# Optimization experiments

Hardware: AMD Instinct MI355X
Metric: run time of the kernel (lower is better)

The kernel has to match this reference:

```python
import jax, jax.numpy as jnp
import numpy as np

DIM = 768
NUM_HEADS = 12
HEAD_DIM = DIM // NUM_HEADS
HW = 32  # input_size = (32, 32)


def setup_inputs() -> dict:
    key = jax.random.key(0)
    ks = jax.random.split(key, 7)
    return {
        "x": jax.random.normal(ks[0], (8, HW, HW, DIM), dtype=jnp.float32),
        "w_qkv": jax.random.normal(ks[1], (DIM, 3 * DIM), dtype=jnp.float32) * 0.02,
        "b_qkv": jnp.zeros((3 * DIM,), dtype=jnp.float32),
        "w_proj": jax.random.normal(ks[2], (DIM, DIM), dtype=jnp.float32) * 0.02,
        "b_proj": jnp.zeros((DIM,), dtype=jnp.float32),
        "rel_pos_h": jax.random.normal(ks[3], (2 * HW - 1, HEAD_DIM), dtype=jnp.float32) * 0.02,
        "rel_pos_w": jax.random.normal(ks[4], (2 * HW - 1, HEAD_DIM), dtype=jnp.float32) * 0.02,
    }


def _gather_rel_pos(size, rel_pos):
    # q_size == k_size == size, so no resize; index = i - j + (size - 1)
    idx = jnp.arange(size)[:, None] - jnp.arange(size)[None, :] + (size - 1)
    return rel_pos[idx]  # [size, size, head_dim]


def reference(x, w_qkv, b_qkv, w_proj, b_proj, rel_pos_h, rel_pos_w):
    B, H, W, C = x.shape
    nH, D = NUM_HEADS, HEAD_DIM
    scale = D ** -0.5
    S = H * W

    qkv = x.reshape(B, S, C) @ w_qkv + b_qkv          # [B,S,3C]
    qkv = qkv.reshape(B, S, 3, nH, D).transpose(2, 0, 3, 1, 4)  # [3,B,nH,S,D]
    q, k, v = qkv[0], qkv[1], qkv[2]

    attn = jnp.einsum('bnsd,bntd->bnst', q * scale, k)  # [B,nH,S,S]

    # decomposed relative positional bias
    Rh = _gather_rel_pos(H, rel_pos_h)                  # [H,H,D]
    Rw = _gather_rel_pos(W, rel_pos_w)                  # [W,W,D]
    r_q = q.reshape(B, nH, H, W, D)
    rel_h = jnp.einsum('bnhwc,hkc->bnhwk', r_q, Rh)     # [B,nH,H,W,H]
    rel_w = jnp.einsum('bnhwc,wkc->bnhwk', r_q, Rw)     # [B,nH,H,W,W]
    attn = (attn.reshape(B, nH, H, W, H, W)
            + rel_h[..., :, None]
            + rel_w[..., None, :]).reshape(B, nH, S, S)

    attn = jax.nn.softmax(attn, axis=-1)
    out = jnp.einsum('bnst,bntd->bnsd', attn, v)        # [B,nH,S,D]
    out = out.transpose(0, 2, 1, 3).reshape(B, H, W, C)
    return out @ w_proj + b_proj
```

## Files before the change

kernel.cpp:

```cpp
#include <hip/hip_runtime.h>
#include <cstdint>
#include <cstddef>

#define NH 12
#define HDIM 64
#define C_ 768
#define C3 2304
#define SEQ 1024
#define LS 72
#define LSV 76
#define SMAX 6.0f
#define LOG2E 1.4426950408889634f

typedef short bf16x8_t __attribute__((ext_vector_type(8)));
typedef float f32x4_t __attribute__((ext_vector_type(4)));
typedef unsigned short u16x4_t __attribute__((ext_vector_type(4)));

__device__ __forceinline__ unsigned short bf16_rne(float x) {
    unsigned int u = __float_as_uint(x);
    u += 0x7FFFu + ((u >> 16) & 1u);
    return (unsigned short)(u >> 16);
}
__device__ __forceinline__ float bf16f(unsigned short h) {
    return __uint_as_float(((unsigned int)h) << 16);
}

__device__ __forceinline__ void load_lds16(const unsigned short* g, unsigned short* l) {
    auto gp = (const __attribute__((address_space(1))) unsigned short*)(uintptr_t)g;
    auto lp = (__attribute__((address_space(3))) unsigned short*)(uint32_t)(uintptr_t)l;
    __builtin_amdgcn_global_load_lds(gp, lp, 16, 0, 0);
}

__device__ __forceinline__ int swz(int row, int g) {
    const int pr = row >> 1;
    const int ch = (((row & 1) << 2) | g) ^ (pr & 7);
    return pr * 64 + ch * 8;
}

__global__ __launch_bounds__(256)
void split_kernel(const float* __restrict__ in, unsigned short* __restrict__ hi)
{
    const int i = blockIdx.x * 256 + threadIdx.x;
    float4 v = ((const float4*)in)[i];
    u16x4_t h;
    h.x = bf16_rne(v.x); h.y = bf16_rne(v.y); h.z = bf16_rne(v.z); h.w = bf16_rne(v.w);
    ((u16x4_t*)hi)[i] = h;
}

__global__ __launch_bounds__(256)
void splitT_kernel(const float* __restrict__ W, unsigned short* __restrict__ Thi,
                   unsigned short* __restrict__ Tlo, int Kdim, int Ndim)
{
    __shared__ float tile[32][33];
    const int t = threadIdx.x;
    const int kb = blockIdx.y * 32, nb = blockIdx.x * 32;
    const int lr = t >> 3, lc = (t & 7) * 4;
    *(float4*)&tile[lr][lc] = *(const float4*)&W[(size_t)(kb + lr) * Ndim + nb + lc];
    __syncthreads();
    const float v0 = tile[lc + 0][lr];
    const float v1 = tile[lc + 1][lr];
    const float v2 = tile[lc + 2][lr];
    const float v3 = tile[lc + 3][lr];
    u16x4_t h, l;
    h.x = bf16_rne(v0); l.x = bf16_rne(v0 - bf16f(h.x));
    h.y = bf16_rne(v1); l.y = bf16_rne(v1 - bf16f(h.y));
    h.z = bf16_rne(v2); l.z = bf16_rne(v2 - bf16f(h.z));
    h.w = bf16_rne(v3); l.w = bf16_rne(v3 - bf16f(h.w));
    *(u16x4_t*)&Thi[(size_t)(nb + lr) * Kdim + kb + lc] = h;
    *(u16x4_t*)&Tlo[(size_t)(nb + lr) * Kdim + kb + lc] = l;
}

__global__ __launch_bounds__(256, 4)
void qkvgemm_kernel(const unsigned short* __restrict__ Ahi, const unsigned short* __restrict__ BThi,
                    const float* __restrict__ bias,
                    unsigned short* __restrict__ q_hi, unsigned short* __restrict__ k_hi,
                    unsigned short* __restrict__ v_hi)
{
    constexpr int K = 768;
    __shared__ unsigned short As[2][4096];
    __shared__ unsigned short Bs[2][4096];
    const int tid = threadIdx.x;
    const int w = tid >> 6, lane = tid & 63, g = lane >> 4, r = lane & 15;
    const int wr = (w >> 1) * 64, wc = (w & 1) * 64;

    const int bid  = blockIdx.x;
    const int xcd  = bid & 7;
    const int idx  = bid >> 3;
    const int msub = idx & 7;
    const int ntile = idx >> 3;
    const int m0 = (xcd * 8 + msub) * 128;
    const int n0 = ntile * 128;

    int row_[2], gc_[2];
#pragma unroll
    for (int i = 0; i < 2; ++i) {
        const int s = i * 256 + tid;
        const int pr = s >> 3;
        const int u = (s & 7) ^ (pr & 7);
        row_[i] = pr * 2 + (u >> 2);
        gc_[i]  = u & 3;
    }
    const unsigned short* gA0 = Ahi + (size_t)(m0 + row_[0]) * K + gc_[0] * 8;
    const unsigned short* gA1 = Ahi + (size_t)(m0 + row_[1]) * K + gc_[1] * 8;
    const unsigned short* gB0 = BThi + (size_t)(n0 + row_[0]) * K + gc_[0] * 8;
    const unsigned short* gB1 = BThi + (size_t)(n0 + row_[1]) * K + gc_[1] * 8;
    const int lofs0 = w * 512;
    const int lofs1 = 2048 + w * 512;

    f32x4_t acc[4][4];
#pragma unroll
    for (int i = 0; i < 4; ++i)
#pragma unroll
        for (int j = 0; j < 4; ++j)
#pragma unroll
            for (int q = 0; q < 4; ++q) acc[i][j][q] = 0.f;

    load_lds16(gA0, &As[0][lofs0]);
    load_lds16(gA1, &As[0][lofs1]);
    load_lds16(gB0, &Bs[0][lofs0]);
    load_lds16(gB1, &Bs[0][lofs1]);

    int cur = 0;
    for (int k0 = 0; k0 < K; k0 += 32) {
        __syncthreads();
        if (k0 + 32 < K) {
            const int nb2 = cur ^ 1;
            load_lds16(gA0 + k0 + 32, &As[nb2][lofs0]);
            load_lds16(gA1 + k0 + 32, &As[nb2][lofs1]);
            load_lds16(gB0 + k0 + 32, &Bs[nb2][lofs0]);
            load_lds16(gB1 + k0 + 32, &Bs[nb2][lofs1]);
        }
        bf16x8_t am[4];
#pragma unroll
        for (int i = 0; i < 4; ++i)
            am[i] = *(const bf16x8_t*)&As[cur][swz(wr + 16 * i + r, g)];
#pragma unroll
        for (int j = 0; j < 4; ++j) {
            const bf16x8_t bn = *(const bf16x8_t*)&Bs[cur][swz(wc + 16 * j + r, g)];
#pragma unroll
            for (int i = 0; i < 4; ++i)
                acc[i][j] = __builtin_amdgcn_mfma_f32_16x16x32_bf16(am[i], bn, acc[i][j], 0, 0, 0);
        }
        cur ^= 1;
    }

    const int third = n0 >= 1536 ? 2 : (n0 >= 768 ? 1 : 0);
    unsigned short* outH = third == 2 ? v_hi : third == 1 ? k_hi : q_hi;
#pragma unroll
    for (int j = 0; j < 4; ++j) {
        const int n = n0 + wc + 16 * j + r;
        const float bj = bias[n];
        const int nn = n - third * 768;
        const int h = nn >> 6, d = nn & 63;
#pragma unroll
        for (int i = 0; i < 4; ++i) {
            const int m = m0 + wr + 16 * i + 4 * g;
            const int b = m >> 10, t = m & 1023;
            const size_t hb = ((size_t)(b * NH + h)) << 16;
            unsigned short* dh = outH + hb + (size_t)t * 64 + d;
#pragma unroll
            for (int q = 0; q < 4; ++q)
                dh[(size_t)q * 64] = bf16_rne(acc[i][j][q] + bj);
        }
    }
}

template<int N>
__global__ __launch_bounds__(256, 2)
void gemm_mfma_kernel(const unsigned short* __restrict__ Ahi, const unsigned short* __restrict__ Alo,
                      const unsigned short* __restrict__ BThi, const unsigned short* __restrict__ BTlo,
                      const float* __restrict__ bias, float* __restrict__ C)
{
    constexpr int K = 768;
    __shared__ unsigned short As[128 * LS];
    __shared__ unsigned short Bs[128 * LS];
    const int tid = threadIdx.x;
    const int w = tid >> 6, lane = tid & 63, g = lane >> 4, r = lane & 15;
    const int wr = (w >> 1) * 64, wc = (w & 1) * 64;

    const int bid  = blockIdx.x;
    const int xcd  = bid & 7;
    const int idx  = bid >> 3;
    const int msub = idx & 7;
    const int ntile = idx >> 3;
    const int m0 = (xcd * 8 + msub) * 128;
    const int n0 = ntile * 128;

    const int srow = tid >> 1, sh = (tid & 1) * 16;

    const unsigned short* aH = Ahi + (size_t)(m0 + srow) * K + sh;
    const unsigned short* aL = Alo + (size_t)(m0 + srow) * K + sh;
    const unsigned short* bH = BThi + (size_t)(n0 + srow) * K + sh;
    const unsigned short* bL = BTlo + (size_t)(n0 + srow) * K + sh;

    f32x4_t acc[4][4];
#pragma unroll
    for (int i = 0; i < 4; ++i)
#pragma unroll
        for (int j = 0; j < 4; ++j)
#pragma unroll
            for (int q = 0; q < 4; ++q) acc[i][j][q] = 0.f;

    for (int k0 = 0; k0 < K; k0 += 32) {
        bf16x8_t va0 = *(const bf16x8_t*)(aH + k0);
        bf16x8_t va1 = *(const bf16x8_t*)(aH + k0 + 8);
        bf16x8_t wa0 = *(const bf16x8_t*)(aL + k0);
        bf16x8_t wa1 = *(const bf16x8_t*)(aL + k0 + 8);
        bf16x8_t vb0 = *(const bf16x8_t*)(bH + k0);
        bf16x8_t vb1 = *(const bf16x8_t*)(bH + k0 + 8);
        bf16x8_t wb0 = *(const bf16x8_t*)(bL + k0);
        bf16x8_t wb1 = *(const bf16x8_t*)(bL + k0 + 8);
        __syncthreads();
        *(bf16x8_t*)&As[srow * LS + sh]          = va0;
        *(bf16x8_t*)&As[srow * LS + sh + 8]      = va1;
        *(bf16x8_t*)&As[srow * LS + 32 + sh]     = wa0;
        *(bf16x8_t*)&As[srow * LS + 32 + sh + 8] = wa1;
        *(bf16x8_t*)&Bs[srow * LS + sh]          = vb0;
        *(bf16x8_t*)&Bs[srow * LS + sh + 8]      = vb1;
        *(bf16x8_t*)&Bs[srow * LS + 32 + sh]     = wb0;
        *(bf16x8_t*)&Bs[srow * LS + 32 + sh + 8] = wb1;
        __syncthreads();
        bf16x8_t amh[4], aml[4];
#pragma unroll
        for (int i = 0; i < 4; ++i) {
            amh[i] = *(const bf16x8_t*)&As[(wr + 16 * i + r) * LS + 8 * g];
            aml[i] = *(const bf16x8_t*)&As[(wr + 16 * i + r) * LS + 32 + 8 * g];
        }
#pragma unroll
        for (int j = 0; j < 4; ++j) {
            bf16x8_t bnh = *(const bf16x8_t*)&Bs[(wc + 16 * j + r) * LS + 8 * g];
            bf16x8_t bnl = *(const bf16x8_t*)&Bs[(wc + 16 * j + r) * LS + 32 + 8 * g];
#pragma unroll
            for (int i = 0; i < 4; ++i) {
                acc[i][j] = __builtin_amdgcn_mfma_f32_16x16x32_bf16(amh[i], bnh, acc[i][j], 0, 0, 0);
                acc[i][j] = __builtin_amdgcn_mfma_f32_16x16x32_bf16(amh[i], bnl, acc[i][j], 0, 0, 0);
                acc[i][j] = __builtin_amdgcn_mfma_f32_16x16x32_bf16(aml[i], bnh, acc[i][j], 0, 0, 0);
            }
        }
    }

#pragma unroll
    for (int j = 0; j < 4; ++j) {
        const float bj = bias[n0 + wc + 16 * j + r];
#pragma unroll
        for (int i = 0; i < 4; ++i) {
            float* Cp = C + (size_t)(m0 + wr + 16 * i + 4 * g) * N + n0 + wc + 16 * j + r;
#pragma unroll
            for (int q = 0; q < 4; ++q)
                Cp[(size_t)q * N] = acc[i][j][q] + bj;
        }
    }
}

__global__ __launch_bounds__(256)
void relcat_kernel(const float* __restrict__ rel_h, const float* __restrict__ rel_w,
                   unsigned short* __restrict__ relcat)
{
    const int i = blockIdx.x * 256 + threadIdx.x;
    if (i >= 2016) return;
    const int j = i * 4;
    const int row = j >> 6, col = j & 63;
    const float* src = row < 63 ? &rel_h[row * 64 + col] : &rel_w[(row - 63) * 64 + col];
    const float4 v = *(const float4*)src;
    u16x4_t h;
    h.x = bf16_rne(v.x); h.y = bf16_rne(v.y); h.z = bf16_rne(v.z); h.w = bf16_rne(v.w);
    *(u16x4_t*)&relcat[j] = h;
}

__global__ __launch_bounds__(256, 4)
void relgemm_kernel(const unsigned short* __restrict__ qhi, const unsigned short* __restrict__ relcat,
                    unsigned short* __restrict__ G)
{
    __shared__ unsigned short bs[128 * LS];
    const int tid = threadIdx.x;
    const int sb = blockIdx.x, bh = blockIdx.y;
    const int w = tid >> 6, lane = tid & 63, g = lane >> 4, r = lane & 15;
    const size_t hb = (size_t)bh << 16;

    {
        const int row = tid >> 1, c32 = (tid & 1) * 32;
        if (row < 126) {
#pragma unroll
            for (int e = 0; e < 4; ++e)
                *(bf16x8_t*)&bs[row * LS + c32 + 8 * e] =
                    *(const bf16x8_t*)&relcat[row * 64 + c32 + 8 * e];
        } else {
            const bf16x8_t z = {0,0,0,0,0,0,0,0};
#pragma unroll
            for (int e = 0; e < 4; ++e)
                *(bf16x8_t*)&bs[row * LS + c32 + 8 * e] = z;
        }
    }
    bf16x8_t aq[2][2];
#pragma unroll
    for (int i = 0; i < 2; ++i)
#pragma unroll
        for (int c = 0; c < 2; ++c)
            aq[i][c] = *(const bf16x8_t*)(qhi + hb + (size_t)(sb * 128 + w * 32 + 16 * i + r) * 64 + c * 32 + 8 * g);
    __syncthreads();

    f32x4_t acc[2][8];
#pragma unroll
    for (int i = 0; i < 2; ++i)
#pragma unroll
        for (int fj = 0; fj < 8; ++fj)
#pragma unroll
            for (int q = 0; q < 4; ++q) acc[i][fj][q] = 0.f;

#pragma unroll
    for (int c = 0; c < 2; ++c)
#pragma unroll
        for (int fj = 0; fj < 8; ++fj) {
            const bf16x8_t brel = *(const bf16x8_t*)&bs[(16 * fj + r) * LS + c * 32 + 8 * g];
#pragma unroll
            for (int i = 0; i < 2; ++i)
                acc[i][fj] = __builtin_amdgcn_mfma_f32_16x16x32_bf16(aq[i][c], brel, acc[i][fj], 0, 0, 0);
        }

    unsigned short* Gb = G + (((size_t)bh << 10) + sb * 128 + w * 32) * 128;
#pragma unroll
    for (int i = 0; i < 2; ++i)
#pragma unroll
        for (int reg = 0; reg < 4; ++reg) {
            unsigned short* Gr = Gb + (size_t)(16 * i + 4 * g + reg) * 128 + r;
#pragma unroll
            for (int fj = 0; fj < 8; ++fj)
                Gr[16 * fj] = bf16_rne(acc[i][fj][reg]);
        }
}

__global__ __launch_bounds__(256, 4)
void attn10_kernel(const unsigned short* __restrict__ qhi,
                   const unsigned short* __restrict__ khi,
                   const unsigned short* __restrict__ vhi,
                   const unsigned short* __restrict__ G,
                   unsigned short* __restrict__ outh, unsigned short* __restrict__ outl)
{
    __shared__ unsigned short ksh[2 * 64 * LS];
    __shared__ unsigned short vsh[2 * 64 * LSV];

    const int tid  = threadIdx.x;
    const int bh   = blockIdx.x;
    const int s0   = blockIdx.y * 64;
    const int w    = tid >> 6;
    const int lane = tid & 63;
    const int g    = lane >> 4;
    const int r    = lane & 15;
    const size_t hb = (size_t)bh << 16;

    bf16x8_t aq[2];
#pragma unroll
    for (int c = 0; c < 2; ++c)
        aq[c] = *(const bf16x8_t*)(qhi + hb + (size_t)(s0 + w * 16 + r) * 64 + c * 32 + 8 * g);

    const unsigned short* Gbh = G + ((size_t)bh << 17);
    const int q    = s0 + w * 16 + r;
    const int qoff = q * 128;
    const int qcb  = (q >> 5) + 31;
    const int iw   = q & 31;
    float bw[4][2];
#pragma unroll
    for (int reg = 0; reg < 4; ++reg)
#pragma unroll
        for (int jh = 0; jh < 2; ++jh)
            bw[reg][jh] = bf16f(Gbh[qoff + 94 + iw - 16 * jh - 4 * g - reg]) * LOG2E;

    f32x4_t oacc[4];
    float lsum[4];
#pragma unroll
    for (int i = 0; i < 4; ++i) {
        lsum[i] = 0.f;
#pragma unroll
        for (int j = 0; j < 4; ++j) oacc[i][j] = 0.f;
    }

    const int krow = tid >> 2, kc16 = (tid & 3) * 16;
    const int tb = (tid >> 4) * 4, d0 = (tid & 15) * 4;
    const int addr_a = (((g & 1) << 5) + r) << 2;
    const int addr_b = addr_a + 64;
    const bool lowg = g < 2;

    {
        const unsigned short* kh = khi + hb + (size_t)krow * 64 + kc16;
        const bf16x8_t a0 = *(const bf16x8_t*)kh;
        const bf16x8_t a1 = *(const bf16x8_t*)(kh + 8);
        u16x4_t rv[4];
#pragma unroll
        for (int i = 0; i < 4; ++i)
            rv[i] = *(const u16x4_t*)(vhi + hb + (size_t)(tb + i) * 64 + d0);
        *(bf16x8_t*)&ksh[krow * LS + kc16]     = a0;
        *(bf16x8_t*)&ksh[krow * LS + kc16 + 8] = a1;
#pragma unroll
        for (int c2 = 0; c2 < 4; ++c2) {
            u16x4_t th;
            th.x = rv[0][c2]; th.y = rv[1][c2]; th.z = rv[2][c2]; th.w = rv[3][c2];
            *(u16x4_t*)&vsh[(d0 + c2) * LSV + tb] = th;
        }
    }
    __syncthreads();

    int cur = 0;
    for (int t0 = 0; t0 < SEQ; t0 += 64) {
        const int cok = cur * 64 * LS;
        const int cov = cur * 64 * LSV;
        const int tn = (t0 + 64 < SEQ) ? t0 + 64 : t0;
        bf16x8_t nk0, nk1;
        u16x4_t nv[4];
        {
            const unsigned short* kh = khi + hb + (size_t)(tn + krow) * 64 + kc16;
            nk0 = *(const bf16x8_t*)kh;
            nk1 = *(const bf16x8_t*)(kh + 8);
#pragma unroll
            for (int i = 0; i < 4; ++i)
                nv[i] = *(const u16x4_t*)(vhi + hb + (size_t)(tn + tb + i) * 64 + d0);
        }

        f32x4_t sacc[4];
#pragma unroll
        for (int fj = 0; fj < 4; ++fj)
#pragma unroll
            for (int j = 0; j < 4; ++j) sacc[fj][j] = 0.f;
#pragma unroll
        for (int c = 0; c < 2; ++c)
#pragma unroll
            for (int fj = 0; fj < 4; ++fj) {
                const bf16x8_t bkh = *(const bf16x8_t*)&ksh[cok + (16 * fj + r) * LS + c * 32 + 8 * g];
                sacc[fj] = __builtin_amdgcn_mfma_f32_16x16x32_bf16(bkh, aq[c], sacc[fj], 0, 0, 0);
            }

        const int kh0 = t0 >> 5;
        const float bh0 = (bf16f(Gbh[qoff + qcb - kh0])     - SMAX) * LOG2E;
        const float bh1 = (bf16f(Gbh[qoff + qcb - kh0 - 1]) - SMAX) * LOG2E;
#pragma unroll
        for (int fj = 0; fj < 4; ++fj)
#pragma unroll
            for (int reg = 0; reg < 4; ++reg) {
                const float s = fmaf(sacc[fj][reg], 0.125f * LOG2E,
                                     ((fj >> 1) ? bh1 : bh0) + bw[reg][fj & 1]);
                const float e = exp2f(s);
                sacc[fj][reg] = e;
                lsum[reg] += e;
            }

        unsigned int pk01[4], pk23[4];
#pragma unroll
        for (int fj = 0; fj < 4; ++fj) {
            asm("v_cvt_pk_bf16_f32 %0, %1, %2" : "=v"(pk01[fj]) : "v"(sacc[fj][0]), "v"(sacc[fj][1]));
            asm("v_cvt_pk_bf16_f32 %0, %1, %2" : "=v"(pk23[fj]) : "v"(sacc[fj][2]), "v"(sacc[fj][3]));
        }

#pragma unroll
        for (int c = 0; c < 2; ++c) {
            const int a01A = __builtin_amdgcn_ds_bpermute(addr_a, (int)pk01[2 * c]);
            const int a23A = __builtin_amdgcn_ds_bpermute(addr_a, (int)pk23[2 * c]);
            const int b01A = __builtin_amdgcn_ds_bpermute(addr_b, (int)pk01[2 * c]);
            const int b23A = __builtin_amdgcn_ds_bpermute(addr_b, (int)pk23[2 * c]);
            const int a01B = __builtin_amdgcn_ds_bpermute(addr_a, (int)pk01[2 * c + 1]);
            const int a23B = __builtin_amdgcn_ds_bpermute(addr_a, (int)pk23[2 * c + 1]);
            const int b01B = __builtin_amdgcn_ds_bpermute(addr_b, (int)pk01[2 * c + 1]);
            const int b23B = __builtin_amdgcn_ds_bpermute(addr_b, (int)pk23[2 * c + 1]);
            union { int u[4]; bf16x8_t v; } pf;
            pf.u[0] = lowg ? a01A : a01B;
            pf.u[1] = lowg ? a23A : a23B;
            pf.u[2] = lowg ? b01A : b01B;
            pf.u[3] = lowg ? b23A : b23B;
#pragma unroll
            for (int fd = 0; fd < 4; ++fd) {
                const bf16x8_t bvh = *(const bf16x8_t*)&vsh[cov + (16 * fd + r) * LSV + c * 32 + 8 * g];
                oacc[fd] = __builtin_amdgcn_mfma_f32_16x16x32_bf16(bvh, pf.v, oacc[fd], 0, 0, 0);
            }
        }

        const int nok = (cur ^ 1) * 64 * LS;
        const int nov = (cur ^ 1) * 64 * LSV;
        *(bf16x8_t*)&ksh[nok + krow * LS + kc16]     = nk0;
        *(bf16x8_t*)&ksh[nok + krow * LS + kc16 + 8] = nk1;
#pragma unroll
        for (int c2 = 0; c2 < 4; ++c2) {
            u16x4_t th;
            th.x = nv[0][c2]; th.y = nv[1][c2]; th.z = nv[2][c2]; th.w = nv[3][c2];
            *(u16x4_t*)&vsh[nov + (d0 + c2) * LSV + tb] = th;
        }
        __syncthreads();
        cur ^= 1;
    }

    const int b = bh / NH, h = bh - (bh / NH) * NH;
    float rs = (lsum[0] + lsum[1]) + (lsum[2] + lsum[3]);
    rs += __shfl_xor(rs, 16);
    rs += __shfl_xor(rs, 32);
    const float rinv = 1.f / rs;
    unsigned short* oph = outh + ((size_t)b * SEQ + q) * C_ + h * HDIM + 4 * g;
    unsigned short* opl = outl + ((size_t)b * SEQ + q) * C_ + h * HDIM + 4 * g;
#pragma unroll
    for (int fd = 0; fd < 4; ++fd) {
        u16x4_t hv, lv;
#pragma unroll
        for (int reg = 0; reg < 4; ++reg) {
            const float v = oacc[fd][reg] * rinv;
            const unsigned short hh = bf16_rne(v);
            hv[reg] = hh;
            lv[reg] = bf16_rne(v - bf16f(hh));
        }
        *(u16x4_t*)(oph + 16 * fd) = hv;
        *(u16x4_t*)(opl + 16 * fd) = lv;
    }
}

extern "C" void kernel_launch(void* const* d_in, const int* in_sizes, int n_in,
                              void* d_out, int out_size, void* d_ws, size_t ws_size,
                              hipStream_t stream) {
    (void)in_sizes; (void)n_in; (void)out_size; (void)ws_size;
    const float* x      = (const float*)d_in[0];
    const float* w_qkv  = (const float*)d_in[1];
    const float* b_qkv  = (const float*)d_in[2];
    const float* w_proj = (const float*)d_in[3];
    const float* b_proj = (const float*)d_in[4];
    const float* rel_h  = (const float*)d_in[5];
    const float* rel_w  = (const float*)d_in[6];
    float* out = (float*)d_out;

    char* base = (char*)d_ws;
    unsigned short* xhi    = (unsigned short*)(base + 0);
    unsigned short* xlo    = (unsigned short*)(base + 12582912);
    unsigned short* wqh    = (unsigned short*)(base + 25165824);
    unsigned short* wql    = (unsigned short*)(base + 28704768);
    unsigned short* wph    = (unsigned short*)(base + 32243712);
    unsigned short* wpl    = (unsigned short*)(base + 33423360);
    unsigned short* qhi    = (unsigned short*)(base + 34603008);
    unsigned short* relcat = (unsigned short*)(base + 47185920);
    unsigned short* khi    = (unsigned short*)(base + 59768832);
    unsigned short* vhi    = (unsigned short*)(base + 84934656);
    unsigned short* G      = (unsigned short*)(base + 110100480);
    unsigned short* ohif   = xhi;
    unsigned short* olo    = xlo;

    split_kernel<<<6144, 256, 0, stream>>>(x, xhi);
    {
        dim3 gq(C3 / 32, C_ / 32);
        splitT_kernel<<<gq, 256, 0, stream>>>(w_qkv, wqh, wql, C_, C3);
        dim3 gp(C_ / 32, C_ / 32);
        splitT_kernel<<<gp, 256, 0, stream>>>(w_proj, wph, wpl, C_, C_);
        relcat_kernel<<<8, 256, 0, stream>>>(rel_h, rel_w, relcat);
    }
    qkvgemm_kernel<<<1152, 256, 0, stream>>>(xhi, wqh, b_qkv, qhi, khi, vhi);
    {
        dim3 grid(8, 96);
        relgemm_kernel<<<grid, 256, 0, stream>>>(qhi, relcat, G);
    }
    {
        dim3 grid(96, SEQ / 64);
        attn10_kernel<<<grid, 256, 0, stream>>>(qhi, khi, vhi, G, ohif, olo);
    }
    gemm_mfma_kernel<C_><<<384, 256, 0, stream>>>(ohif, olo, wph, wpl, b_proj, out);
}
```

Before: 175.7 us.

## Fuse prep kernels, double-buffer proj GEMM with async LDS loads, add setprio

Merges the four preprocessing kernels (x bf16 cast, two weight split-transposes, rel-pos concat) into one launch dispatched by block index, removing three launch gaps. The projection GEMM switches from register-staged single-buffered LDS to double-buffered global_load_lds with the swizzled layout used by the QKV GEMM, so the next K tile loads while MFMAs run. s_setprio is raised around the MFMA blocks in the QKV GEMM, attention and projection kernels. The costs are higher LDS use in the projection GEMM, which may lower occupancy, and more divergent block roles in the prep kernel.

Result: faster. 166.8 us (-5.0%).

```diff
diff --git a/kernel.cpp b/kernel.cpp
--- a/kernel.cpp
+++ b/kernel.cpp
@@ -37,23 +37,12 @@
     return pr * 64 + ch * 8;
 }
 
-__global__ __launch_bounds__(256)
-void split_kernel(const float* __restrict__ in, unsigned short* __restrict__ hi)
+__device__ __forceinline__ void splitT_body(const float* __restrict__ W,
+                                            unsigned short* __restrict__ Thi,
+                                            unsigned short* __restrict__ Tlo,
+                                            int Kdim, int Ndim, int kb, int nb,
+                                            float (*tile)[33], int t)
 {
-    const int i = blockIdx.x * 256 + threadIdx.x;
-    float4 v = ((const float4*)in)[i];
-    u16x4_t h;
-    h.x = bf16_rne(v.x); h.y = bf16_rne(v.y); h.z = bf16_rne(v.z); h.w = bf16_rne(v.w);
-    ((u16x4_t*)hi)[i] = h;
-}
-
-__global__ __launch_bounds__(256)
-void splitT_kernel(const float* __restrict__ W, unsigned short* __restrict__ Thi,
-                   unsigned short* __restrict__ Tlo, int Kdim, int Ndim)
-{
-    __shared__ float tile[32][33];
-    const int t = threadIdx.x;
-    const int kb = blockIdx.y * 32, nb = blockIdx.x * 32;
     const int lr = t >> 3, lc = (t & 7) * 4;
     *(float4*)&tile[lr][lc] = *(const float4*)&W[(size_t)(kb + lr) * Ndim + nb + lc];
     __syncthreads();
@@ -70,6 +59,45 @@
     *(u16x4_t*)&Tlo[(size_t)(nb + lr) * Kdim + kb + lc] = l;
 }
 
+__global__ __launch_bounds__(256)
+void prep_kernel(const float* __restrict__ x, const float* __restrict__ w_qkv,
+                 const float* __restrict__ w_proj,
+                 const float* __restrict__ rel_h, const float* __restrict__ rel_w,
+                 unsigned short* __restrict__ xhi,
+                 unsigned short* __restrict__ wqh, unsigned short* __restrict__ wql,
+                 unsigned short* __restrict__ wph, unsigned short* __restrict__ wpl,
+                 unsigned short* __restrict__ relcat)
+{
+    __shared__ float tile[32][33];
+    const int bid = blockIdx.x, tid = threadIdx.x;
+    if (bid < 6144) {
+        const int i = bid * 256 + tid;
+        float4 v = ((const float4*)x)[i];
+        u16x4_t h;
+        h.x = bf16_rne(v.x); h.y = bf16_rne(v.y); h.z = bf16_rne(v.z); h.w = bf16_rne(v.w);
+        ((u16x4_t*)xhi)[i] = h;
+    } else if (bid < 7872) {
+        const int local = bid - 6144;
+        const int bx = local % 72, by = local / 72;
+        splitT_body(w_qkv, wqh, wql, C_, C3, by * 32, bx * 32, tile, tid);
+    } else if (bid < 8448) {
+        const int local = bid - 7872;
+        const int bx = local % 24, by = local / 24;
+        splitT_body(w_proj, wph, wpl, C_, C_, by * 32, bx * 32, tile, tid);
+    } else {
+        const int i = (bid - 8448) * 256 + tid;
+        if (i < 2016) {
+            const int j = i * 4;
+            const int row = j >> 6, col = j & 63;
+            const float* src = row < 63 ? &rel_h[row * 64 + col] : &rel_w[(row - 63) * 64 + col];
+            const float4 v = *(const float4*)src;
+            u16x4_t h;
+            h.x = bf16_rne(v.x); h.y = bf16_rne(v.y); h.z = bf16_rne(v.z); h.w = bf16_rne(v.w);
+            *(u16x4_t*)&relcat[j] = h;
+        }
+    }
+}
+
 __global__ __launch_bounds__(256, 4)
 void qkvgemm_kernel(const unsigned short* __restrict__ Ahi, const unsigned short* __restrict__ BThi,
                     const float* __restrict__ bias,
@@ -134,6 +162,7 @@
 #pragma unroll
         for (int i = 0; i < 4; ++i)
             am[i] = *(const bf16x8_t*)&As[cur][swz(wr + 16 * i + r, g)];
+        __builtin_amdgcn_s_setprio(1);
 #pragma unroll
         for (int j = 0; j < 4; ++j) {
             const bf16x8_t bn = *(const bf16x8_t*)&Bs[cur][swz(wc + 16 * j + r, g)];
@@ -141,6 +170,7 @@
             for (int i = 0; i < 4; ++i)
                 acc[i][j] = __builtin_amdgcn_mfma_f32_16x16x32_bf16(am[i], bn, acc[i][j], 0, 0, 0);
         }
+        __builtin_amdgcn_s_setprio(0);
         cur ^= 1;
     }
 
@@ -165,15 +195,15 @@
     }
 }
 
-template<int N>
 __global__ __launch_bounds__(256, 2)
-void gemm_mfma_kernel(const unsigned short* __restrict__ Ahi, const unsigned short* __restrict__ Alo,
-                      const unsigned short* __restrict__ BThi, const unsigned short* __restrict__ BTlo,
-                      const float* __restrict__ bias, float* __restrict__ C)
+void projgemm_kernel(const unsigned short* __restrict__ Ahi, const unsigned short* __restrict__ Alo,
+                     const unsigned short* __restrict__ BThi, const unsigned short* __restrict__ BTlo,
+                     const float* __restrict__ bias, float* __restrict__ C)
 {
     constexpr int K = 768;
-    __shared__ unsigned short As[128 * LS];
-    __shared__ unsigned short Bs[128 * LS];
+    constexpr int N = C_;
+    __shared__ unsigned short Ash[2][4096], Asl[2][4096];
+    __shared__ unsigned short Bsh[2][4096], Bsl[2][4096];
     const int tid = threadIdx.x;
     const int w = tid >> 6, lane = tid & 63, g = lane >> 4, r = lane & 15;
     const int wr = (w >> 1) * 64, wc = (w & 1) * 64;
@@ -186,12 +216,25 @@
     const int m0 = (xcd * 8 + msub) * 128;
     const int n0 = ntile * 128;
 
-    const int srow = tid >> 1, sh = (tid & 1) * 16;
-
-    const unsigned short* aH = Ahi + (size_t)(m0 + srow) * K + sh;
-    const unsigned short* aL = Alo + (size_t)(m0 + srow) * K + sh;
-    const unsigned short* bH = BThi + (size_t)(n0 + srow) * K + sh;
-    const unsigned short* bL = BTlo + (size_t)(n0 + srow) * K + sh;
+    int row_[2], gc_[2];
+#pragma unroll
+    for (int i = 0; i < 2; ++i) {
+        const int s = i * 256 + tid;
+        const int pr = s >> 3;
+        const int u = (s & 7) ^ (pr & 7);
+        row_[i] = pr * 2 + (u >> 2);
+        gc_[i]  = u & 3;
+    }
+    const unsigned short* gAh0 = Ahi + (size_t)(m0 + row_[0]) * K + gc_[0] * 8;
+    const unsigned short* gAh1 = Ahi + (size_t)(m0 + row_[1]) * K + gc_[1] * 8;
+    const unsigned short* gAl0 = Alo + (size_t)(m0 + row_[0]) * K + gc_[0] * 8;
+    const unsigned short* gAl1 = Alo + (size_t)(m0 + row_[1]) * K + gc_[1] * 8;
+    const unsigned short* gBh0 = BThi + (size_t)(n0 + row_[0]) * K + gc_[0] * 8;
+    const unsigned short* gBh1 = BThi + (size_t)(n0 + row_[1]) * K + gc_[1] * 8;
+    const unsigned short* gBl0 = BTlo + (size_t)(n0 + row_[0]) * K + gc_[0] * 8;
+    const unsigned short* gBl1 = BTlo + (size_t)(n0 + row_[1]) * K + gc_[1] * 8;
+    const int lofs0 = w * 512;
+    const int lofs1 = 2048 + w * 512;
 
     f32x4_t acc[4][4];
 #pragma unroll
@@ -201,35 +244,42 @@
 #pragma unroll
             for (int q = 0; q < 4; ++q) acc[i][j][q] = 0.f;
 
+    load_lds16(gAh0, &Ash[0][lofs0]);
+    load_lds16(gAh1, &Ash[0][lofs1]);
+    load_lds16(gAl0, &Asl[0][lofs0]);
+    load_lds16(gAl1, &Asl[0][lofs1]);
+    load_lds16(gBh0, &Bsh[0][lofs0]);
+    load_lds16(gBh1, &Bsh[0][lofs1]);
+    load_lds16(gBl0, &Bsl[0][lofs0]);
+    load_lds16(gBl1, &Bsl[0][lofs1]);
+
+    int cur = 0;
     for (int k0 = 0; k0 < K; k0 += 32) {
-        bf16x8_t va0 = *(const bf16x8_t*)(aH + k0);
-        bf16x8_t va1 = *(const bf16x8_t*)(aH + k0 + 8);
-        bf16x8_t wa0 = *(const bf16x8_t*)(aL + k0);
-        bf16x8_t wa1 = *(const bf16x8_t*)(aL + k0 + 8);
-        bf16x8_t vb0 = *(const bf16x8_t*)(bH + k0);
-        bf16x8_t vb1 = *(const bf16x8_t*)(bH + k0 + 8);
-        bf16x8_t wb0 = *(const bf16x8_t*)(bL + k0);
-        bf16x8_t wb1 = *(const bf16x8_t*)(bL + k0 + 8);
         __syncthreads();
-        *(bf16x8_t*)&As[srow * LS + sh]          = va0;
-        *(bf16x8_t*)&As[srow * LS + sh + 8]      = va1;
-        *(bf16x8_t*)&As[srow * LS + 32 + sh]     = wa0;
-        *(bf16x8_t*)&As[srow * LS + 32 + sh + 8] = wa1;
-        *(bf16x8_t*)&Bs[srow * LS + sh]          = vb0;
-        *(bf16x8_t*)&Bs[srow * LS + sh + 8]      = vb1;
-        *(bf16x8_t*)&Bs[srow * LS + 32 + sh]     = wb0;
-        *(bf16x8_t*)&Bs[srow * LS + 32 + sh + 8] = wb1;
-        __syncthreads();
+        if (k0 + 32 < K) {
+            const int nb2 = cur ^ 1;
+            load_lds16(gAh0 + k0 + 32, &Ash[nb2][lofs0]);
+            load_lds16(gAh1 + k0 + 32, &Ash[nb2][lofs1]);
+            load_lds16(gAl0 + k0 + 32, &Asl[nb2][lofs0]);
+            load_lds16(gAl1 + k0 + 32, &Asl[nb2][lofs1]);
+            load_lds16(gBh0 + k0 + 32, &Bsh[nb2][lofs0]);
+            load_lds16(gBh1 + k0 + 32, &Bsh[nb2][lofs1]);
+            load_lds16(gBl0 + k0 + 32, &Bsl[nb2][lofs0]);
+            load_lds16(gBl1 + k0 + 32, &Bsl[nb2][lofs1]);
+        }
         bf16x8_t amh[4], aml[4];
 #pragma unroll
         for (int i = 0; i < 4; ++i) {
-            amh[i] = *(const bf16x8_t*)&As[(wr + 16 * i + r) * LS + 8 * g];
-            aml[i] = *(const bf16x8_t*)&As[(wr + 16 * i + r) * LS + 32 + 8 * g];
-        }
+            const int o = swz(wr + 16 * i + r, g);
+            amh[i] = *(const bf16x8_t*)&Ash[cur][o];
+            aml[i] = *(const bf16x8_t*)&Asl[cur][o];
+        }
+        __builtin_amdgcn_s_setprio(1);
 #pragma unroll
         for (int j = 0; j < 4; ++j) {
-            bf16x8_t bnh = *(const bf16x8_t*)&Bs[(wc + 16 * j + r) * LS + 8 * g];
-            bf16x8_t bnl = *(const bf16x8_t*)&Bs[(wc + 16 * j + r) * LS + 32 + 8 * g];
+            const int o = swz(wc + 16 * j + r, g);
+            const bf16x8_t bnh = *(const bf16x8_t*)&Bsh[cur][o];
+            const bf16x8_t bnl = *(const bf16x8_t*)&Bsl[cur][o];
 #pragma unroll
             for (int i = 0; i < 4; ++i) {
                 acc[i][j] = __builtin_amdgcn_mfma_f32_16x16x32_bf16(amh[i], bnh, acc[i][j], 0, 0, 0);
@@ -237,6 +287,8 @@
                 acc[i][j] = __builtin_amdgcn_mfma_f32_16x16x32_bf16(aml[i], bnh, acc[i][j], 0, 0, 0);
             }
         }
+        __builtin_amdgcn_s_setprio(0);
+        cur ^= 1;
     }
 
 #pragma unroll
@@ -250,21 +302,6 @@
                 Cp[(size_t)q * N] = acc[i][j][q] + bj;
         }
     }
-}
-
-__global__ __launch_bounds__(256)
-void relcat_kernel(const float* __restrict__ rel_h, const float* __restrict__ rel_w,
-                   unsigned short* __restrict__ relcat)
-{
-    const int i = blockIdx.x * 256 + threadIdx.x;
-    if (i >= 2016) return;
-    const int j = i * 4;
-    const int row = j >> 6, col = j & 63;
-    const float* src = row < 63 ? &rel_h[row * 64 + col] : &rel_w[(row - 63) * 64 + col];
-    const float4 v = *(const float4*)src;
-    u16x4_t h;
-    h.x = bf16_rne(v.x); h.y = bf16_rne(v.y); h.z = bf16_rne(v.z); h.w = bf16_rne(v.w);
-    *(u16x4_t*)&relcat[j] = h;
 }
 
 __global__ __launch_bounds__(256, 4)
@@ -330,7 +367,7 @@
 }
 
 __global__ __launch_bounds__(256, 4)
-void attn10_kernel(const unsigned short* __restrict__ qhi,
+void attn11_kernel(const unsigned short* __restrict__ qhi,
                    const unsigned short* __restrict__ khi,
                    const unsigned short* __restrict__ vhi,
                    const unsigned short* __restrict__ G,
@@ -420,6 +457,7 @@
         for (int fj = 0; fj < 4; ++fj)
 #pragma unroll
             for (int j = 0; j < 4; ++j) sacc[fj][j] = 0.f;
+        __builtin_amdgcn_s_setprio(1);
 #pragma unroll
         for (int c = 0; c < 2; ++c)
 #pragma unroll
@@ -427,6 +465,7 @@
                 const bf16x8_t bkh = *(const bf16x8_t*)&ksh[cok + (16 * fj + r) * LS + c * 32 + 8 * g];
                 sacc[fj] = __builtin_amdgcn_mfma_f32_16x16x32_bf16(bkh, aq[c], sacc[fj], 0, 0, 0);
             }
+        __builtin_amdgcn_s_setprio(0);
 
         const int kh0 = t0 >> 5;
         const float bh0 = (bf16f(Gbh[qoff + qcb - kh0])     - SMAX) * LOG2E;
@@ -464,11 +503,13 @@
             pf.u[1] = lowg ? a23A : a23B;
             pf.u[2] = lowg ? b01A : b01B;
             pf.u[3] = lowg ? b23A : b23B;
+            __builtin_amdgcn_s_setprio(1);
 #pragma unroll
             for (int fd = 0; fd < 4; ++fd) {
                 const bf16x8_t bvh = *(const bf16x8_t*)&vsh[cov + (16 * fd + r) * LSV + c * 32 + 8 * g];
                 oacc[fd] = __builtin_amdgcn_mfma_f32_16x16x32_bf16(bvh, pf.v, oacc[fd], 0, 0, 0);
             }
+            __builtin_amdgcn_s_setprio(0);
         }
 
         const int nok = (cur ^ 1) * 64 * LS;
@@ -535,14 +576,8 @@
     unsigned short* ohif   = xhi;
     unsigned short* olo    = xlo;
 
-    split_kernel<<<6144, 256, 0, stream>>>(x, xhi);
-    {
-        dim3 gq(C3 / 32, C_ / 32);
-        splitT_kernel<<<gq, 256, 0, stream>>>(w_qkv, wqh, wql, C_, C3);
-        dim3 gp(C_ / 32, C_ / 32);
-        splitT_kernel<<<gp, 256, 0, stream>>>(w_proj, wph, wpl, C_, C_);
-        relcat_kernel<<<8, 256, 0, stream>>>(rel_h, rel_w, relcat);
-    }
+    prep_kernel<<<8456, 256, 0, stream>>>(x, w_qkv, w_proj, rel_h, rel_w,
+                                          xhi, wqh, wql, wph, wpl, relcat);
     qkvgemm_kernel<<<1152, 256, 0, stream>>>(xhi, wqh, b_qkv, qhi, khi, vhi);
     {
         dim3 grid(8, 96);
@@ -550,7 +585,7 @@
     }
     {
         dim3 grid(96, SEQ / 64);
-        attn10_kernel<<<grid, 256, 0, stream>>>(qhi, khi, vhi, G, ohif, olo);
-    }
-    gemm_mfma_kernel<C_><<<384, 256, 0, stream>>>(ohif, olo, wph, wpl, b_proj, out);
-}
+        attn11_kernel<<<grid, 256, 0, stream>>>(qhi, khi, vhi, G, ohif, olo);
+    }
+    projgemm_kernel<<<384, 256, 0, stream>>>(ohif, olo, wph, wpl, b_proj, out);
+}
```
